# Optimization experiments

Hardware: AMD Instinct MI355X
Metric: run time of the kernel (lower is better)

Reference implementation:

```python
import jax, jax.numpy as jnp
import numpy as np
import math


def _sph_harm(l_max, cos_theta, phi):
    """Real spherical harmonics Y_l^m for l=0..l_max.

    Returns a tuple of arrays, one per l, each of shape [N, 2l+1] with
    columns ordered m = -l..l. Uses the standard associated-Legendre
    recurrences (with Condon-Shortley phase inside P_l^m) and the real
    orthonormal convention:
      m<0: sqrt(2)*K* P_l^{|m|}(x) * sin(|m| phi)
      m=0:          K* P_l^0(x)
      m>0: sqrt(2)*K* P_l^{m}(x)   * cos(m phi)
    with K = sqrt((2l+1)/(4pi) * (l-|m|)!/(l+|m|)!).
    """
    x = cos_theta
    s = jnp.sqrt(jnp.clip(1.0 - x * x, 0.0, 1.0))  # sin(theta) >= 0

    # Associated Legendre polynomials via recurrence, vectorized over N.
    P = {(0, 0): jnp.ones_like(x)}
    for m in range(1, l_max + 1):
        # P_m^m = -(2m-1) * sin(theta) * P_{m-1}^{m-1}   (Condon-Shortley)
        P[(m, m)] = (-(2 * m - 1)) * s * P[(m - 1, m - 1)]
    for m in range(0, l_max):
        # P_{m+1}^m = (2m+1) * x * P_m^m
        P[(m + 1, m)] = (2 * m + 1) * x * P[(m, m)]
    for m in range(0, l_max + 1):
        for l in range(m + 2, l_max + 1):
            # (l-m) P_l^m = (2l-1) x P_{l-1}^m - (l+m-1) P_{l-2}^m
            P[(l, m)] = ((2 * l - 1) * x * P[(l - 1, m)]
                         - (l + m - 1) * P[(l - 2, m)]) / (l - m)

    sqrt2 = float(np.sqrt(2.0))
    outputs = []
    for l in range(l_max + 1):
        cols = []
        for m in range(-l, l + 1):
            am = abs(m)
            K = float(math.sqrt((2 * l + 1) / (4.0 * math.pi)
                                * math.factorial(l - am) / math.factorial(l + am)))
            if m < 0:
                cols.append((sqrt2 * K) * P[(l, am)] * jnp.sin(am * phi))
            elif m == 0:
                cols.append(K * P[(l, 0)])
            else:
                cols.append((sqrt2 * K) * P[(l, m)] * jnp.cos(m * phi))
        outputs.append(jnp.stack(cols, axis=1))  # [N, 2l+1]
    return tuple(outputs)


def setup_inputs() -> dict:
    key = jax.random.key(0)
    k1, k2 = jax.random.split(key)
    N = 2_000_000
    cos_theta = jax.random.uniform(k1, (N,), dtype=jnp.float32,
                                   minval=-1.0, maxval=1.0)
    phi = jax.random.uniform(k2, (N,), dtype=jnp.float32,
                             minval=-np.pi, maxval=np.pi)
    return {"cos_theta": cos_theta, "phi": phi, "l_max": 7}


def reference(cos_theta, phi, l_max):
    return _sph_harm(l_max, cos_theta, phi)
```

## Files before the change

### kernel.cpp

```cpp
#include <hip/hip_runtime.h>
#include <hip/hip_bf16.h>


#define BLOCK 128
#define LSTRIDE 65

static constexpr double kfac(int l, int m) {
    double f = 1.0;
    for (int k = l - m + 1; k <= l + m; ++k) f *= (double)k;
    return f;
}

__global__ __launch_bounds__(BLOCK) void sph_harm_f32(
    const float* __restrict__ ct, const float* __restrict__ ph,
    float* __restrict__ out, int N)
{
    __shared__ float lds[BLOCK * LSTRIDE];

    const int tid = threadIdx.x;
    const int bp0 = blockIdx.x * BLOCK;
    const int P_blk = min(BLOCK, N - bp0);

    if (tid < P_blk) {
        const int n = bp0 + tid;
        const float x = ct[n];
        const float p = ph[n];
        float s2 = 1.0f - x * x;
        s2 = s2 < 0.0f ? 0.0f : s2;
        const float st = sqrtf(s2);

        float s1, c1;
        sincosf(p, &s1, &c1);
        float cm[8], sm[8];
        cm[0] = 1.0f; sm[0] = 0.0f;
#pragma unroll
        for (int m = 1; m <= 7; ++m) {
            cm[m] = cm[m - 1] * c1 - sm[m - 1] * s1;
            sm[m] = sm[m - 1] * c1 + cm[m - 1] * s1;
        }

        float Pa[8][8];
        Pa[0][0] = 1.0f;
#pragma unroll
        for (int m = 1; m <= 7; ++m)
            Pa[m][m] = (float)(-(2 * m - 1)) * st * Pa[m - 1][m - 1];
#pragma unroll
        for (int m = 0; m <= 6; ++m)
            Pa[m + 1][m] = (float)(2 * m + 1) * x * Pa[m][m];
#pragma unroll
        for (int m = 0; m <= 7; ++m) {
#pragma unroll
            for (int l = m + 2; l <= 7; ++l) {
                Pa[l][m] = ((float)(2 * l - 1) * x * Pa[l - 1][m]
                            - (float)(l + m - 1) * Pa[l - 2][m])
                           / (float)(l - m);
            }
        }

        float* row = &lds[tid * LSTRIDE];
        const double INV4PI = 0.07957747154594767;
        const float SQRT2 = 1.4142135623730951f;
#pragma unroll
        for (int l = 0; l <= 7; ++l) {
            const float K0 = sqrtf((float)((double)(2 * l + 1) * INV4PI));
            row[l * l + l] = K0 * Pa[l][0];
#pragma unroll
            for (int m = 1; m <= l; ++m) {
                const float Km = sqrtf(
                    (float)((double)(2 * l + 1) * INV4PI / kfac(l, m)));
                const float base = SQRT2 * Km * Pa[l][m];
                row[l * l + (l - m)] = base * sm[m];
                row[l * l + (l + m)] = base * cm[m];
            }
        }
    }
    __syncthreads();

    const size_t NN = (size_t)N;
#pragma unroll
    for (int l = 0; l <= 7; ++l) {
        const int w = 2 * l + 1;
        const int ll = l * l;
        float* cbase = out + NN * (size_t)ll + (size_t)bp0 * (size_t)w;
        const int cnt = P_blk * w;
        for (int e = tid; e < cnt; e += BLOCK) {
            const int q = e / w;
            const int r = e - q * w;
            cbase[e] = lds[q * LSTRIDE + ll + r];
        }
    }
}

extern "C" void kernel_launch(void* const* d_in, const int* in_sizes, int n_in,
                              void* d_out, int out_size, void* d_ws, size_t ws_size,
                              hipStream_t stream) {
    const float* ct = (const float*)d_in[0];
    const float* ph = (const float*)d_in[1];
    float* out = (float*)d_out;
    const int N = in_sizes[0];
    const int blocks = (N + BLOCK - 1) / BLOCK;
    hipLaunchKernelGGL(sph_harm_f32, dim3(blocks), dim3(BLOCK), 0, stream,
                       ct, ph, out, N);
}
```

Baseline: 528.9 us.

## Stream harmonics per degree through double-buffered LDS with vectorized float4 stores

Restructures the kernel so each degree l is computed with a rolling two-row Legendre recurrence and written into one of two small LDS buffers. The buffer for the previous degree is copied to global memory as float4 while the next degree is computed. This cuts LDS use from 65 floats per thread to two 15-float buffers, raising occupancy (launch bounds now request 4 blocks), and removes the per-element integer division in the store loop. The Y00 column is written directly as a constant. In exchange it adds a barrier per degree, and the float4 path relies on 16-byte alignment of each output slice.

```diff
diff --git a/kernel.cpp b/kernel.cpp
--- a/kernel.cpp
+++ b/kernel.cpp
@@ -3,7 +3,8 @@
 
 
 #define BLOCK 128
-#define LSTRIDE 65
+#define MAXW 15
+#define BUFSZ (BLOCK * MAXW)
 
 static constexpr double kfac(int l, int m) {
     double f = 1.0;
@@ -11,82 +12,121 @@
     return f;
 }
 
-__global__ __launch_bounds__(BLOCK) void sph_harm_f32(
+__global__ __launch_bounds__(BLOCK, 4) void sph_harm_f32(
     const float* __restrict__ ct, const float* __restrict__ ph,
     float* __restrict__ out, int N)
 {
-    __shared__ float lds[BLOCK * LSTRIDE];
+    __shared__ __align__(16) float buf[2][BUFSZ];
 
     const int tid = threadIdx.x;
     const int bp0 = blockIdx.x * BLOCK;
     const int P_blk = min(BLOCK, N - bp0);
+    const bool full = (P_blk == BLOCK);
+    const bool act = (tid < P_blk);
 
-    if (tid < P_blk) {
-        const int n = bp0 + tid;
-        const float x = ct[n];
-        const float p = ph[n];
-        float s2 = 1.0f - x * x;
-        s2 = s2 < 0.0f ? 0.0f : s2;
-        const float st = sqrtf(s2);
+    const int n = bp0 + (act ? tid : 0);
+    const float x = ct[n];
+    const float p = ph[n];
+    float s2 = 1.0f - x * x;
+    s2 = s2 < 0.0f ? 0.0f : s2;
+    const float st = sqrtf(s2);
 
-        float s1, c1;
-        sincosf(p, &s1, &c1);
-        float cm[8], sm[8];
-        cm[0] = 1.0f; sm[0] = 0.0f;
+    const float Y00 = 0.28209479177387814f;
+    if (full) {
+        if (tid < BLOCK / 4) {
+            float4 v; v.x = Y00; v.y = Y00; v.z = Y00; v.w = Y00;
+            reinterpret_cast<float4*>(out + bp0)[tid] = v;
+        }
+    } else {
+        for (int e = tid; e < P_blk; e += BLOCK) out[bp0 + e] = Y00;
+    }
+
+    float s1, c1;
+    sincosf(p, &s1, &c1);
+    float cm[8], sm[8];
+    cm[0] = 1.0f; sm[0] = 0.0f;
 #pragma unroll
-        for (int m = 1; m <= 7; ++m) {
-            cm[m] = cm[m - 1] * c1 - sm[m - 1] * s1;
-            sm[m] = sm[m - 1] * c1 + cm[m - 1] * s1;
-        }
+    for (int m = 1; m <= 7; ++m) {
+        cm[m] = cm[m - 1] * c1 - sm[m - 1] * s1;
+        sm[m] = sm[m - 1] * c1 + cm[m - 1] * s1;
+    }
 
-        float Pa[8][8];
-        Pa[0][0] = 1.0f;
+    const double INV4PI = 0.07957747154594767;
+    const float SQRT2 = 1.4142135623730951f;
+
+    float pp[8], pr[8], cur[8];
+    pr[0] = 1.0f;
+
 #pragma unroll
-        for (int m = 1; m <= 7; ++m)
-            Pa[m][m] = (float)(-(2 * m - 1)) * st * Pa[m - 1][m - 1];
+    for (int l = 1; l <= 7; ++l) {
+        const int w = 2 * l + 1;
+
 #pragma unroll
-        for (int m = 0; m <= 6; ++m)
-            Pa[m + 1][m] = (float)(2 * m + 1) * x * Pa[m][m];
-#pragma unroll
-        for (int m = 0; m <= 7; ++m) {
-#pragma unroll
-            for (int l = m + 2; l <= 7; ++l) {
-                Pa[l][m] = ((float)(2 * l - 1) * x * Pa[l - 1][m]
-                            - (float)(l + m - 1) * Pa[l - 2][m])
-                           / (float)(l - m);
-            }
-        }
+        for (int m = 0; m <= l - 2; ++m)
+            cur[m] = ((float)(2 * l - 1) * x * pr[m]
+                      - (float)(l + m - 1) * pp[m]) / (float)(l - m);
+        cur[l - 1] = (float)(2 * l - 1) * x * pr[l - 1];
+        cur[l]     = (float)(-(2 * l - 1)) * st * pr[l - 1];
 
-        float* row = &lds[tid * LSTRIDE];
-        const double INV4PI = 0.07957747154594767;
-        const float SQRT2 = 1.4142135623730951f;
-#pragma unroll
-        for (int l = 0; l <= 7; ++l) {
+        if (act) {
+            float* b = &buf[l & 1][tid * w];
             const float K0 = sqrtf((float)((double)(2 * l + 1) * INV4PI));
-            row[l * l + l] = K0 * Pa[l][0];
+            b[l] = K0 * cur[0];
 #pragma unroll
             for (int m = 1; m <= l; ++m) {
                 const float Km = sqrtf(
                     (float)((double)(2 * l + 1) * INV4PI / kfac(l, m)));
-                const float base = SQRT2 * Km * Pa[l][m];
-                row[l * l + (l - m)] = base * sm[m];
-                row[l * l + (l + m)] = base * cm[m];
+                const float base = SQRT2 * Km * cur[m];
+                b[l - m] = base * sm[m];
+                b[l + m] = base * cm[m];
             }
         }
+
+        if (l >= 2) {
+            const int lc = l - 1, wc = 2 * lc + 1;
+            const float* sb = buf[lc & 1];
+            float* dst = out + (size_t)N * (size_t)(lc * lc)
+                         + (size_t)bp0 * (size_t)wc;
+            if (full) {
+                const float4* s4 = reinterpret_cast<const float4*>(sb);
+                float4* d4 = reinterpret_cast<float4*>(dst);
+                const int cnt4 = 32 * wc;
+#pragma unroll
+                for (int k = 0; k * BLOCK < cnt4; ++k) {
+                    const int e = tid + k * BLOCK;
+                    if ((k + 1) * BLOCK <= cnt4 || e < cnt4) d4[e] = s4[e];
+                }
+            } else {
+                const int cnt = P_blk * wc;
+                for (int e = tid; e < cnt; e += BLOCK) dst[e] = sb[e];
+            }
+        }
+
+        __syncthreads();
+
+#pragma unroll
+        for (int m = 0; m <= l - 1; ++m) pp[m] = pr[m];
+#pragma unroll
+        for (int m = 0; m <= l; ++m) pr[m] = cur[m];
     }
-    __syncthreads();
 
-    const size_t NN = (size_t)N;
+    {
+        const int lc = 7, wc = 15;
+        const float* sb = buf[lc & 1];
+        float* dst = out + (size_t)N * (size_t)(lc * lc)
+                     + (size_t)bp0 * (size_t)wc;
+        if (full) {
+            const float4* s4 = reinterpret_cast<const float4*>(sb);
+            float4* d4 = reinterpret_cast<float4*>(dst);
+            const int cnt4 = 32 * wc;
 #pragma unroll
-    for (int l = 0; l <= 7; ++l) {
-        const int w = 2 * l + 1;
-        const int ll = l * l;
-        float* cbase = out + NN * (size_t)ll + (size_t)bp0 * (size_t)w;
-        const int cnt = P_blk * w;
-        for (int e = tid; e < cnt; e += BLOCK) {
-            const int q = e / w;
-            const int r = e - q * w;
-            cbase[e] = lds[q * LSTRIDE + ll + r];
+            for (int k = 0; k * BLOCK < cnt4; ++k) {
+                const int e = tid + k * BLOCK;
+                if ((k + 1) * BLOCK <= cnt4 || e < cnt4) d4[e] = s4[e];
+            }
+        } else {
+            const int cnt = P_blk * wc;
+            for (int e = tid; e < cnt; e += BLOCK) dst[e] = sb[e];
         }
     }
 }
```

Result: faster. 509.7 us (-3.6%).
